# Optimization experiments

Hardware: AMD Instinct MI355X
Metric: run time of the kernel (lower is better)

The kernel has to match this reference:

```python
import jax, jax.numpy as jnp
import numpy as np

B, N, E, T, DIN, H, G, ND, NT, L = 4, 10000, 320000, 16, 16, 64, 64, 16, 3, 7


def _mlp2(x, W1, b1, W2, b2):
    # Linear -> LeakyReLU -> (Dropout: eval identity) -> Linear -> LeakyReLU
    h = jax.nn.leaky_relu(x @ W1 + b1)
    return jax.nn.leaky_relu(h @ W2 + b2)


def _gcn_conv(x, src, dst, ew, nt, W1, b1, W2, b2):
    # x: [B,N,D], nt: [B,N,ND], ew: [*,E,1] broadcastable over batch
    x_in = _mlp2(jnp.concatenate([x, nt], axis=-1), W1, b1, W2, b2)  # [B,N,G]
    msgs = x_in[:, src, :] * ew                                      # gather + weight, [B,E,G]
    aggr = jnp.zeros(x_in.shape, x_in.dtype).at[:, dst, :].add(msgs) # scatter-add, [B,N,G]
    return x + aggr


def _gru(x, Wx, Wh, bx, bh):
    # PyTorch-style GRU over time axis. x: [B,N,T,DIN] -> hs: [T,B,N,H]
    xw = jnp.einsum('bntd,dh->tbnh', x, Wx) + bx  # precompute input projections [T,B,N,3H]
    h0 = jnp.zeros(x.shape[:2] + (Wh.shape[0],), x.dtype)

    def step(h, xw_t):
        hw = h @ Wh + bh
        xr, xz, xn = jnp.split(xw_t, 3, axis=-1)
        hr, hz, hn = jnp.split(hw, 3, axis=-1)
        r = jax.nn.sigmoid(xr + hr)
        z = jax.nn.sigmoid(xz + hz)
        n = jnp.tanh(xn + r * hn)
        h_new = (1 - z) * n + z * h
        return h_new, h_new

    _, hs = jax.lax.scan(step, h0, xw)
    return hs


def reference(input_day, edge_attr, gru_Wx, gru_Wh, gru_bx, gru_bh,
              rnn_fc_W, rnn_fc_b,
              e_emb, e_c0_W1, e_c0_b1, e_c0_W2, e_c0_b2,
              e_c1_W1, e_c1_b1, e_c1_W2, e_c1_b2,
              e_fm_W1, e_fm_b1, e_fm_W2, e_fm_b2,
              g_emb, g_c0_W1, g_c0_b1, g_c0_W2, g_c0_b2,
              g_c1_W1, g_c1_b1, g_c1_W2, g_c1_b2,
              gcn_fc_W, gcn_fc_b,
              edge_index, node_type_ids):
    src, dst = edge_index[0], edge_index[1]

    # KRNN encoder (GRU) + max over time + FC head
    hs = _gru(input_day, gru_Wx, gru_Wh, gru_bx, gru_bh)  # [T,B,N,H]
    rnn_out = hs.max(axis=0)                              # kr_out.max(dim=-2) -> [B,N,H]
    y_rnn = rnn_out @ rnn_fc_W + rnn_fc_b                 # [B,N,L]

    # EdgeNet: GCN stack on static edge_attr, then per-edge pair MLP -> gate
    nt_e = jnp.broadcast_to(e_emb[node_type_ids][None], (B, N, ND))
    ew0 = edge_attr.reshape(1, E, 1)
    x = rnn_out
    x = _gcn_conv(x, src, dst, ew0, nt_e, e_c0_W1, e_c0_b1, e_c0_W2, e_c0_b2)
    x = _gcn_conv(x, src, dst, ew0, nt_e, e_c1_W1, e_c1_b1, e_c1_W2, e_c1_b2)
    edge_x = jnp.concatenate([x[:, src, :], x[:, dst, :]], axis=-1)  # [B,E,2G]
    h = jax.nn.leaky_relu(edge_x @ e_fm_W1 + e_fm_b1)
    edge_gate = jax.nn.relu(h @ e_fm_W2 + e_fm_b2)                   # [B,E,1]

    # Main GCNNet with learned edge gates
    nt_g = jnp.broadcast_to(g_emb[node_type_ids][None], (B, N, ND))
    x = rnn_out
    x = _gcn_conv(x, src, dst, edge_gate, nt_g, g_c0_W1, g_c0_b1, g_c0_W2, g_c0_b2)
    x = _gcn_conv(x, src, dst, edge_gate, nt_g, g_c1_W1, g_c1_b1, g_c1_W2, g_c1_b2)
    y_gcn = x @ gcn_fc_W + gcn_fc_b                                  # [B,N,L]

    return y_rnn + y_gcn


def setup_inputs() -> dict:
    key = jax.random.key(0)
    ks = iter(jax.random.split(key, 48))

    def nrm(shape, s=0.1):
        return jax.random.normal(next(ks), shape, jnp.float32) * s

    inp = {}
    inp['input_day'] = jax.random.normal(next(ks), (B, N, T, DIN), jnp.float32)
    inp['edge_index'] = jax.random.randint(next(ks), (2, E), 0, N)
    inp['node_type_ids'] = jax.random.randint(next(ks), (N,), 0, NT)
    inp['edge_attr'] = jax.random.uniform(next(ks), (E,), jnp.float32)

    inp['gru_Wx'] = nrm((DIN, 3 * H))
    inp['gru_Wh'] = nrm((H, 3 * H))
    inp['gru_bx'] = jnp.zeros((3 * H,), jnp.float32)
    inp['gru_bh'] = jnp.zeros((3 * H,), jnp.float32)
    inp['rnn_fc_W'] = nrm((H, L))
    inp['rnn_fc_b'] = jnp.zeros((L,), jnp.float32)

    inp['e_emb'] = nrm((NT, ND))
    inp['g_emb'] = nrm((NT, ND))
    for pre, in_dim in (('e_c0', H + ND), ('e_c1', G + ND), ('g_c0', H + ND), ('g_c1', G + ND)):
        inp[pre + '_W1'] = nrm((in_dim, G))
        inp[pre + '_b1'] = jnp.zeros((G,), jnp.float32)
        inp[pre + '_W2'] = nrm((G, G))
        inp[pre + '_b2'] = jnp.zeros((G,), jnp.float32)

    inp['e_fm_W1'] = nrm((2 * G, G))
    inp['e_fm_b1'] = jnp.zeros((G,), jnp.float32)
    inp['e_fm_W2'] = nrm((G, 1))
    inp['e_fm_b2'] = jnp.zeros((1,), jnp.float32)

    inp['gcn_fc_W'] = nrm((G, L))
    inp['gcn_fc_b'] = jnp.zeros((L,), jnp.float32)
    return inp
```

## Files before the change

### kernel.cpp

```cpp
#include <hip/hip_runtime.h>
#include <hip/hip_bf16.h>

#define NB 4
#define NN 10000
#define NE 320000
#define BN 40000
#define NL 7

typedef float f32x4 __attribute__((ext_vector_type(4)));
typedef __bf16 bf16x8 __attribute__((ext_vector_type(8)));

__device__ __forceinline__ float bf2f(unsigned short u){
  unsigned x = ((unsigned)u) << 16;
  return __builtin_bit_cast(float, x);
}
__device__ __forceinline__ unsigned short f2bf(float f){
  unsigned u = __builtin_bit_cast(unsigned, f);
  u += 0x7fffu + ((u >> 16) & 1u);
  return (unsigned short)(u >> 16);
}
__device__ __forceinline__ bf16x8 zero8(){
  uint4 z = make_uint4(0u,0u,0u,0u);
  return __builtin_bit_cast(bf16x8, z);
}
__device__ __forceinline__ bf16x8 one8(){
  uint4 z = make_uint4(0x3f80u,0u,0u,0u);
  return __builtin_bit_cast(bf16x8, z);
}
__device__ __forceinline__ bf16x8 ld8bf(const unsigned short* p){
  uint4 u = *(const uint4*)p;
  return __builtin_bit_cast(bf16x8, u);
}
__device__ __forceinline__ unsigned pk2(float lo, float hi){
  unsigned r;
  asm("v_cvt_pk_bf16_f32 %0, %1, %2" : "=v"(r) : "v"(lo), "v"(hi));
  return r;
}
__device__ __forceinline__ bf16x8 ld8f(const float* p){
  float4 a = *(const float4*)p;
  float4 b = *(const float4*)(p+4);
  uint4 u = make_uint4(pk2(a.x,a.y), pk2(a.z,a.w), pk2(b.x,b.y), pk2(b.z,b.w));
  return __builtin_bit_cast(bf16x8, u);
}
__device__ __forceinline__ float frcp(float x){ return __builtin_amdgcn_rcpf(x); }
__device__ __forceinline__ float tanh_(float x){ return 1.f - 2.f*frcp(__expf(2.f*x)+1.f); }
__device__ __forceinline__ float lrelu(float x){ return x > 0.f ? x : 0.01f*x; }

#define LDS_WAIT() asm volatile("s_waitcnt lgkmcnt(0)" ::: "memory")

__device__ __forceinline__ void mlp2_body(
    int bid,
    const float* __restrict__ x,
    const int* __restrict__ ntid,
    const float* __restrict__ emb,
    const float* __restrict__ W1,
    const float* __restrict__ b1,
    const float* __restrict__ W2,
    const float* __restrict__ b2,
    unsigned short* __restrict__ out)
{
  __shared__ __attribute__((aligned(16))) unsigned short W1T[64][96];
  __shared__ __attribute__((aligned(16))) unsigned short W2T[64][72];
  __shared__ __attribute__((aligned(16))) unsigned short hb[4][16][72];
  __shared__ float sb1[64], sb2[64];
  int tid = threadIdx.x;
  for (int i=tid;i<80*64;i+=256){ int k=i>>6, n=i&63; W1T[n][k]=f2bf(W1[i]); }
  for (int i=tid;i<64*16;i+=256){ int n=i>>4, k=80+(i&15); W1T[n][k]=0; }
  for (int i=tid;i<64*64;i+=256){ int k=i>>6, n=i&63; W2T[n][k]=f2bf(W2[i]); }
  if (tid<64){ sb1[tid]=b1[tid]; sb2[tid]=b2[tid]; }
  __syncthreads();

  int wave = tid>>6, lane = tid&63, ln16 = lane&15, quad = lane>>4;
  int row0 = bid*64 + wave*16;
  int r_ = row0 + ln16;
  const float* xr = x + (size_t)r_*64;
  bf16x8 a0 = ld8f(xr + quad*8);
  bf16x8 a1 = ld8f(xr + 32 + quad*8);
  int id = ntid[r_ % NN];
  bf16x8 a2 = (quad<2) ? ld8f(emb + id*16 + quad*8) : zero8();

  f32x4 acc[4];
  #pragma unroll
  for (int nt=0;nt<4;++nt){
    float bb = sb1[nt*16+ln16];
    acc[nt] = (f32x4){bb,bb,bb,bb};
    acc[nt] = __builtin_amdgcn_mfma_f32_16x16x32_bf16(a0, ld8bf(&W1T[nt*16+ln16][quad*8]),    acc[nt], 0,0,0);
    acc[nt] = __builtin_amdgcn_mfma_f32_16x16x32_bf16(a1, ld8bf(&W1T[nt*16+ln16][32+quad*8]), acc[nt], 0,0,0);
    acc[nt] = __builtin_amdgcn_mfma_f32_16x16x32_bf16(a2, ld8bf(&W1T[nt*16+ln16][64+quad*8]), acc[nt], 0,0,0);
  }
  #pragma unroll
  for (int nt=0;nt<4;++nt)
    #pragma unroll
    for (int i=0;i<4;++i)
      hb[wave][quad*4+i][nt*16+ln16] = f2bf(lrelu(acc[nt][i]));
  LDS_WAIT();
  bf16x8 h0 = ld8bf(&hb[wave][ln16][quad*8]);
  bf16x8 h1 = ld8bf(&hb[wave][ln16][32+quad*8]);
  f32x4 acc2[4];
  #pragma unroll
  for (int nt=0;nt<4;++nt){
    float bb = sb2[nt*16+ln16];
    acc2[nt] = (f32x4){bb,bb,bb,bb};
    acc2[nt] = __builtin_amdgcn_mfma_f32_16x16x32_bf16(h0, ld8bf(&W2T[nt*16+ln16][quad*8]),    acc2[nt], 0,0,0);
    acc2[nt] = __builtin_amdgcn_mfma_f32_16x16x32_bf16(h1, ld8bf(&W2T[nt*16+ln16][32+quad*8]), acc2[nt], 0,0,0);
  }
  #pragma unroll
  for (int nt=0;nt<4;++nt)
    #pragma unroll
    for (int i=0;i<4;++i)
      out[(size_t)(row0+quad*4+i)*64 + nt*16+ln16] = f2bf(lrelu(acc2[nt][i]));
}

__global__ __launch_bounds__(256, 2) void gru_count_kernel(
    const float* __restrict__ xd,
    const float* __restrict__ Wx,
    const float* __restrict__ Wh,
    const float* __restrict__ bx,
    const float* __restrict__ bh,
    float* __restrict__ rnn,
    const int* __restrict__ ei,
    int* __restrict__ counts)
{
  if (blockIdx.x >= 625){
    int e = (blockIdx.x-625)*256 + threadIdx.x;
    atomicAdd(&counts[ei[NE+e]], 1);
    return;
  }
  __shared__ __attribute__((aligned(16))) unsigned short WhT[192][72];
  __shared__ __attribute__((aligned(16))) unsigned short WxT[192][40];
  __shared__ __attribute__((aligned(16))) unsigned short hb[4][16][76];
  int tid = threadIdx.x;
  int wave = tid >> 6, lane = tid & 63;
  int ln16 = lane & 15, quad = lane >> 4;

  for (int i = tid; i < 64*192; i += 256){
    int k = i / 192, n = i - k*192;
    WhT[n][k] = f2bf(Wh[i]);
  }
  for (int i = tid; i < 16*192; i += 256){
    int k = i / 192, n = i - k*192;
    WxT[n][k] = f2bf(Wx[i]);
    WxT[n][17+k] = 0;
  }
  if (tid < 192){
    float bias = (tid < 128) ? (bx[tid] + bh[tid]) : bx[tid];
    WxT[tid][16] = f2bf(bias);
  }
  for (int i = tid; i < 4*16*76; i += 256) ((unsigned short*)hb)[i] = 0;
  __syncthreads();

  int rowbase = blockIdx.x * 64 + wave * 16;

  bf16x8 whf[2][12];
  #pragma unroll
  for (int kt=0; kt<2; ++kt)
    #pragma unroll
    for (int nt=0; nt<12; ++nt)
      whf[kt][nt] = ld8bf(&WhT[nt*16 + ln16][kt*32 + quad*8]);

  f32x4 bhn2[4];
  #pragma unroll
  for (int j=0;j<4;++j)
    bhn2[j] = *(const f32x4*)(bh + 128 + j*16 + quad*4);

  f32x4 hprev[4], vmax[4];
  #pragma unroll
  for (int j=0;j<4;++j){
    hprev[j] = (f32x4){0.f,0.f,0.f,0.f};
    vmax[j]  = (f32x4){-1e30f,-1e30f,-1e30f,-1e30f};
  }

  const float* xrow = xd + (size_t)(rowbase + ln16) * 256;
  unsigned short* hrow = &hb[wave][ln16][0];

  bf16x8 axc;
  if (quad < 2) axc = ld8f(xrow + quad*8);
  else          axc = (quad == 2) ? one8() : zero8();

  for (int t = 0; t < 16; ++t){
    bf16x8 axn;
    if (quad < 2) axn = (t < 15) ? ld8f(xrow + (t+1)*16 + quad*8) : zero8();
    else          axn = (quad == 2) ? one8() : zero8();
    bf16x8 ah0 = ld8bf(hrow + quad*8);
    bf16x8 ah1 = ld8bf(hrow + 32 + quad*8);

    #pragma unroll
    for (int j=0;j<4;++j){
      bf16x8 xr = ld8bf(&WxT[j*16+ln16][quad*8]);
      bf16x8 xz = ld8bf(&WxT[(4+j)*16+ln16][quad*8]);
      bf16x8 xn = ld8bf(&WxT[(8+j)*16+ln16][quad*8]);
      f32x4 z4 = (f32x4){0.f,0.f,0.f,0.f};
      f32x4 ar = __builtin_amdgcn_mfma_f32_16x16x32_bf16(xr, axc, z4, 0,0,0);
      ar = __builtin_amdgcn_mfma_f32_16x16x32_bf16(whf[0][j], ah0, ar, 0,0,0);
      ar = __builtin_amdgcn_mfma_f32_16x16x32_bf16(whf[1][j], ah1, ar, 0,0,0);
      f32x4 az = __builtin_amdgcn_mfma_f32_16x16x32_bf16(xz, axc, z4, 0,0,0);
      az = __builtin_amdgcn_mfma_f32_16x16x32_bf16(whf[0][4+j], ah0, az, 0,0,0);
      az = __builtin_amdgcn_mfma_f32_16x16x32_bf16(whf[1][4+j], ah1, az, 0,0,0);
      f32x4 an = __builtin_amdgcn_mfma_f32_16x16x32_bf16(xn, axc, z4, 0,0,0);
      f32x4 ah = __builtin_amdgcn_mfma_f32_16x16x32_bf16(whf[0][8+j], ah0, bhn2[j], 0,0,0);
      ah = __builtin_amdgcn_mfma_f32_16x16x32_bf16(whf[1][8+j], ah1, ah, 0,0,0);
      f32x4 hv;
      #pragma unroll
      for (int i=0;i<4;++i){
        float Er = __expf(-ar[i]);
        float Ez = __expf(-az[i]);
        float pr = 1.f + Er, pz = 1.f + Ez;
        float D  = frcp(pr * pz);
        float r  = D * pz;
        float z  = D * pr;
        float nn = tanh_(an[i] + r * ah[i]);
        float h  = fmaf(z, hprev[j][i]-nn, nn);
        hprev[j][i] = h;
        vmax[j][i] = fmaxf(vmax[j][i], h);
        hv[i] = h;
      }
      *(uint2*)&hb[wave][ln16][j*16+quad*4] = make_uint2(pk2(hv[0],hv[1]), pk2(hv[2],hv[3]));
    }
    LDS_WAIT();
    axc = axn;
  }
  float* orow = rnn + (size_t)(rowbase + ln16)*64;
  #pragma unroll
  for (int j=0;j<4;++j)
    *(f32x4*)(orow + j*16 + quad*4) = vmax[j];
}

__global__ __launch_bounds__(1024) void scan_kernel(const int* __restrict__ counts,
                                                    int* __restrict__ rowptr, int* __restrict__ cursor){
  __shared__ int incl[10240];
  __shared__ int wsum[16];
  int tid=threadIdx.x, wave=tid>>6, lane=tid&63;
  int base = wave*640;
  int carry=0;
  #pragma unroll
  for (int c=0;c<10;++c){
    int i = base + c*64 + lane;
    int v = (i<NN)? counts[i] : 0;
    int s = v;
    #pragma unroll
    for (int off=1;off<64;off<<=1){
      int t_ = __shfl_up(s, off);
      if (lane>=off) s += t_;
    }
    s += carry;
    incl[base + c*64 + lane] = s;
    carry = __shfl(s, 63);
  }
  if (lane==63) wsum[wave]=carry;
  __syncthreads();
  if (wave==0){
    int w_ = (lane<16)? wsum[lane]:0;
    #pragma unroll
    for (int off=1;off<16;off<<=1){
      int t_ = __shfl_up(w_, off);
      if (lane>=off) w_ += t_;
    }
    if (lane<16) wsum[lane]=w_;
  }
  __syncthreads();
  int woff = (wave>0)? wsum[wave-1] : 0;
  #pragma unroll
  for (int c=0;c<10;++c){
    int i = base + c*64 + lane;
    if (i<NN){
      int excl = incl[i] + woff - counts[i];
      rowptr[i]=excl; cursor[i]=excl;
    }
  }
  if (tid==0) rowptr[NN]=wsum[15];
}

__global__ __launch_bounds__(256) void fill_mlp2e_kernel(
    const int* __restrict__ ei,
    const float* __restrict__ ea,
    int* __restrict__ cursor,
    int* __restrict__ ssrc,
    float* __restrict__ wcsr,
    const float* __restrict__ x,
    const int* __restrict__ ntid,
    const float* __restrict__ emb,
    const float* __restrict__ W1, const float* __restrict__ b1,
    const float* __restrict__ W2, const float* __restrict__ b2,
    unsigned short* __restrict__ out)
{
  if (blockIdx.x >= 625){
    int e = (blockIdx.x-625)*256 + threadIdx.x;
    int d = ei[NE+e];
    int pos = atomicAdd(&cursor[d],1);
    ssrc[pos]=ei[e];
    wcsr[pos]=ea[e];
    return;
  }
  mlp2_body(blockIdx.x, x, ntid, emb, W1, b1, W2, b2, out);
}

__global__ __launch_bounds__(256) void aggr_mlp_kernel(
    const float* __restrict__ x,
    const unsigned short* __restrict__ xin,
    const int* __restrict__ rowptr,
    const int* __restrict__ ssrc,
    const float* __restrict__ wp,
    int bstride,
    const int* __restrict__ ntid,
    const float* __restrict__ emb,
    const float* __restrict__ W1,
    const float* __restrict__ b1,
    const float* __restrict__ W2,
    const float* __restrict__ b2,
    float* __restrict__ xe_out,
    unsigned short* __restrict__ out)
{
  int u = blockIdx.x;
  int b = (u & 7) >> 1;
  int m = ((u >> 3) << 1) | (u & 1);
  if (m >= 625) return;
  int row0 = b*NN + m*16;

  __shared__ __attribute__((aligned(16))) unsigned short W1T[64][96];
  __shared__ __attribute__((aligned(16))) unsigned short W2T[64][72];
  __shared__ __attribute__((aligned(16))) unsigned short hb[16][72];
  __shared__ __attribute__((aligned(16))) unsigned short h2[16][72];
  __shared__ float sb1[64], sb2[64];
  int tid = threadIdx.x;
  for (int i=tid;i<80*64;i+=256){ int k=i>>6, n=i&63; W1T[n][k]=f2bf(W1[i]); }
  for (int i=tid;i<64*16;i+=256){ int n=i>>4, k=80+(i&15); W1T[n][k]=0; }
  for (int i=tid;i<64*64;i+=256){ int k=i>>6, n=i&63; W2T[n][k]=f2bf(W2[i]); }
  if (tid<64){ sb1[tid]=b1[tid]; sb2[tid]=b2[tid]; }

  int wave = tid>>6, lane = tid&63, ln16 = lane&15, quad = lane>>4;
  int r = wave*4 + quad;
  int row = row0 + r;
  int n = m*16 + r;
  int l = ln16;
  int p0 = rowptr[n], p1 = rowptr[n+1];
  const unsigned short* xb_ = xin + (size_t)b*NN*64;
  const float* wb = wp + (size_t)b*bstride;
  float a0=0.f, a1=0.f, a2=0.f, a3=0.f;
  #pragma unroll 4
  for (int p=p0; p<p1; ++p){
    int s = ssrc[p];
    float w = wb[p];
    uint2 mm = *(const uint2*)(xb_ + (size_t)s*64 + l*4);
    a0 += bf2f((unsigned short)(mm.x & 0xffffu)) * w;
    a1 += bf2f((unsigned short)(mm.x >> 16)) * w;
    a2 += bf2f((unsigned short)(mm.y & 0xffffu)) * w;
    a3 += bf2f((unsigned short)(mm.y >> 16)) * w;
  }
  float4 base = *(const float4*)(x + (size_t)row*64 + l*4);
  float o0=base.x+a0, o1=base.y+a1, o2=base.z+a2, o3=base.w+a3;
  float4 ov; ov.x=o0; ov.y=o1; ov.z=o2; ov.w=o3;
  *(float4*)(xe_out + (size_t)row*64 + l*4) = ov;
  *(uint2*)&hb[r][l*4] = make_uint2(pk2(o0,o1), pk2(o2,o3));
  __syncthreads();

  int id = ntid[m*16 + ln16];
  bf16x8 xa0 = ld8bf(&hb[ln16][quad*8]);
  bf16x8 xa1 = ld8bf(&hb[ln16][32+quad*8]);
  bf16x8 xa2 = (quad<2) ? ld8f(emb + id*16 + quad*8) : zero8();
  float bb = sb1[wave*16+ln16];
  f32x4 acc = (f32x4){bb,bb,bb,bb};
  acc = __builtin_amdgcn_mfma_f32_16x16x32_bf16(xa0, ld8bf(&W1T[wave*16+ln16][quad*8]),    acc, 0,0,0);
  acc = __builtin_amdgcn_mfma_f32_16x16x32_bf16(xa1, ld8bf(&W1T[wave*16+ln16][32+quad*8]), acc, 0,0,0);
  acc = __builtin_amdgcn_mfma_f32_16x16x32_bf16(xa2, ld8bf(&W1T[wave*16+ln16][64+quad*8]), acc, 0,0,0);
  #pragma unroll
  for (int i=0;i<4;++i)
    h2[quad*4+i][wave*16+ln16] = f2bf(lrelu(acc[i]));
  __syncthreads();
  bf16x8 hh0 = ld8bf(&h2[ln16][quad*8]);
  bf16x8 hh1 = ld8bf(&h2[ln16][32+quad*8]);
  float b2v = sb2[wave*16+ln16];
  f32x4 acc2 = (f32x4){b2v,b2v,b2v,b2v};
  acc2 = __builtin_amdgcn_mfma_f32_16x16x32_bf16(hh0, ld8bf(&W2T[wave*16+ln16][quad*8]),    acc2, 0,0,0);
  acc2 = __builtin_amdgcn_mfma_f32_16x16x32_bf16(hh1, ld8bf(&W2T[wave*16+ln16][32+quad*8]), acc2, 0,0,0);
  #pragma unroll
  for (int i=0;i<4;++i)
    out[(size_t)(row0+quad*4+i)*64 + wave*16+ln16] = f2bf(lrelu(acc2[i]));
}

__global__ __launch_bounds__(256) void aggr_uv_kernel(
    const float* __restrict__ x,
    const unsigned short* __restrict__ xin,
    const int* __restrict__ rowptr,
    const int* __restrict__ ssrc,
    const float* __restrict__ wp,
    int bstride,
    const float* __restrict__ W1,
    unsigned short* __restrict__ uvp)
{
  int u = blockIdx.x;
  int b = (u & 7) >> 1;
  int m = ((u >> 3) << 1) | (u & 1);
  if (m >= 625) return;
  int row0 = b*NN + m*16;

  __shared__ __attribute__((aligned(16))) unsigned short WT[128][72];
  __shared__ __attribute__((aligned(16))) unsigned short hb[16][72];
  int tid = threadIdx.x;
  for (int i=tid;i<64*64;i+=256){
    int k=i>>6, n=i&63;
    WT[n][k]    = f2bf(W1[i]);
    WT[64+n][k] = f2bf(W1[64*64 + i]);
  }

  int wave = tid>>6, lane = tid&63, ln16 = lane&15, quad = lane>>4;
  int r = wave*4 + quad;
  int row = row0 + r;
  int n = m*16 + r;
  int l = ln16;
  int p0 = rowptr[n], p1 = rowptr[n+1];
  const unsigned short* xb_ = xin + (size_t)b*NN*64;
  const float* wb = wp + (size_t)b*bstride;
  float a0=0.f, a1=0.f, a2=0.f, a3=0.f;
  #pragma unroll 4
  for (int p=p0; p<p1; ++p){
    int s = ssrc[p];
    float w = wb[p];
    uint2 mm = *(const uint2*)(xb_ + (size_t)s*64 + l*4);
    a0 += bf2f((unsigned short)(mm.x & 0xffffu)) * w;
    a1 += bf2f((unsigned short)(mm.x >> 16)) * w;
    a2 += bf2f((unsigned short)(mm.y & 0xffffu)) * w;
    a3 += bf2f((unsigned short)(mm.y >> 16)) * w;
  }
  float4 base = *(const float4*)(x + (size_t)row*64 + l*4);
  float o0=base.x+a0, o1=base.y+a1, o2=base.z+a2, o3=base.w+a3;
  *(uint2*)&hb[r][l*4] = make_uint2(pk2(o0,o1), pk2(o2,o3));
  __syncthreads();

  bf16x8 xa0 = ld8bf(&hb[ln16][quad*8]);
  bf16x8 xa1 = ld8bf(&hb[ln16][32+quad*8]);
  #pragma unroll
  for (int t=0;t<2;++t){
    int nt = wave*2 + t;
    f32x4 acc = (f32x4){0.f,0.f,0.f,0.f};
    acc = __builtin_amdgcn_mfma_f32_16x16x32_bf16(xa0, ld8bf(&WT[nt*16+ln16][quad*8]),    acc, 0,0,0);
    acc = __builtin_amdgcn_mfma_f32_16x16x32_bf16(xa1, ld8bf(&WT[nt*16+ln16][32+quad*8]), acc, 0,0,0);
    #pragma unroll
    for (int i=0;i<4;++i)
      uvp[(size_t)(row0+quad*4+i)*128 + nt*16+ln16] = f2bf(acc[i]);
  }
}

__global__ __launch_bounds__(256) void gate_mlp2g_kernel(
    const unsigned short* __restrict__ uvp,
    const int* __restrict__ rowptr,
    const int* __restrict__ ssrc,
    const float* __restrict__ b1,
    const float* __restrict__ W2g,
    const float* __restrict__ b2,
    float* __restrict__ gate,
    const float* __restrict__ x,
    const int* __restrict__ ntid,
    const float* __restrict__ emb,
    const float* __restrict__ mW1, const float* __restrict__ mb1,
    const float* __restrict__ mW2, const float* __restrict__ mb2,
    unsigned short* __restrict__ mout)
{
  if (blockIdx.x < 625){
    mlp2_body(blockIdx.x, x, ntid, emb, mW1, mb1, mW2, mb2, mout);
    return;
  }
  int u = blockIdx.x;
  int b = (u & 7) >> 1;
  int m = (((u - 625) >> 3) << 1) | (u & 1);
  if (m >= 2500) return;
  int tid=threadIdx.x;
  int wave=tid>>6, lane=tid&63;
  int sub=lane>>4, l=lane&15;
  int n = m*4 + wave;
  int p0 = rowptr[n], p1 = rowptr[n+1];
  const unsigned short* ub = uvp + (size_t)b*NN*128;
  uint2 vu = *(const uint2*)(ub + (size_t)n*128 + 64 + l*4);
  float v0=bf2f((unsigned short)(vu.x&0xffffu)), v1=bf2f((unsigned short)(vu.x>>16));
  float v2=bf2f((unsigned short)(vu.y&0xffffu)), v3=bf2f((unsigned short)(vu.y>>16));
  float4 bb = *(const float4*)(b1 + l*4);
  float4 ww = *(const float4*)(W2g + l*4);
  float b2v = b2[0];
  float* gb = gate + (size_t)b*NE;
  #pragma unroll 4
  for (int p=p0+sub; p<p1; p+=4){
    int s = ssrc[p];
    uint2 uu = *(const uint2*)(ub + (size_t)s*128 + l*4);
    float h0 = lrelu(bf2f((unsigned short)(uu.x&0xffffu)) + v0 + bb.x);
    float h1 = lrelu(bf2f((unsigned short)(uu.x>>16))     + v1 + bb.y);
    float h2 = lrelu(bf2f((unsigned short)(uu.y&0xffffu)) + v2 + bb.z);
    float h3 = lrelu(bf2f((unsigned short)(uu.y>>16))     + v3 + bb.w);
    float part = h0*ww.x + h1*ww.y + h2*ww.z + h3*ww.w;
    part += __shfl_xor(part,1);
    part += __shfl_xor(part,2);
    part += __shfl_xor(part,4);
    part += __shfl_xor(part,8);
    if (l==0){
      float g = part + b2v;
      gb[p] = g>0.f ? g : 0.f;
    }
  }
}

__global__ __launch_bounds__(256) void aggr_final_kernel(
    const float* x,
    const unsigned short* __restrict__ xin,
    const int* __restrict__ rowptr,
    const int* __restrict__ ssrc,
    const float* __restrict__ wp,
    const float* __restrict__ rnn,
    const float* __restrict__ Wr, const float* __restrict__ br,
    const float* __restrict__ Wg, const float* __restrict__ bg,
    float* __restrict__ out)
{
  int u = blockIdx.x;
  int b = (u & 7) >> 1;
  int m = ((u >> 3) << 1) | (u & 1);
  if (m >= 2500) return;

  __shared__ float sWr[448], sWg[448], sb[7];
  int tid=threadIdx.x;
  for (int i=tid;i<448;i+=256){ sWr[i]=Wr[i]; sWg[i]=Wg[i]; }
  if (tid<7) sb[tid]=br[tid]+bg[tid];
  __syncthreads();
  int wave=tid>>6, lane=tid&63;
  int sub=lane>>4, l=lane&15;
  int n = m*4 + wave;
  int bid = b*NN + n;
  int p0 = rowptr[n], p1 = rowptr[n+1];
  const unsigned short* xb_ = xin + (size_t)b*NN*64;
  const float* wb = wp + (size_t)b*NE;
  float a0=0.f, a1=0.f, a2=0.f, a3=0.f;
  #pragma unroll 4
  for (int p=p0+sub; p<p1; p+=4){
    int s = ssrc[p];
    float w = wb[p];
    uint2 mm = *(const uint2*)(xb_ + (size_t)s*64 + l*4);
    a0 += bf2f((unsigned short)(mm.x & 0xffffu)) * w;
    a1 += bf2f((unsigned short)(mm.x >> 16)) * w;
    a2 += bf2f((unsigned short)(mm.y & 0xffffu)) * w;
    a3 += bf2f((unsigned short)(mm.y >> 16)) * w;
  }
  a0 += __shfl_xor(a0,16); a0 += __shfl_xor(a0,32);
  a1 += __shfl_xor(a1,16); a1 += __shfl_xor(a1,32);
  a2 += __shfl_xor(a2,16); a2 += __shfl_xor(a2,32);
  a3 += __shfl_xor(a3,16); a3 += __shfl_xor(a3,32);
  if (sub==0){
    float4 base = *(const float4*)(x + (size_t)bid*64 + l*4);
    float o0=base.x+a0, o1=base.y+a1, o2=base.z+a2, o3=base.w+a3;
    float4 rr = *(const float4*)(rnn + (size_t)bid*64 + l*4);
    float part[7];
    #pragma unroll
    for (int q=0;q<7;++q)
      part[q] = o0*sWg[(l*4+0)*7+q] + o1*sWg[(l*4+1)*7+q]
              + o2*sWg[(l*4+2)*7+q] + o3*sWg[(l*4+3)*7+q]
              + rr.x*sWr[(l*4+0)*7+q] + rr.y*sWr[(l*4+1)*7+q]
              + rr.z*sWr[(l*4+2)*7+q] + rr.w*sWr[(l*4+3)*7+q];
    #pragma unroll
    for (int q=0;q<7;++q){
      part[q] += __shfl_xor(part[q],1);
      part[q] += __shfl_xor(part[q],2);
      part[q] += __shfl_xor(part[q],4);
      part[q] += __shfl_xor(part[q],8);
    }
    if (l==0){
      #pragma unroll
      for (int q=0;q<7;++q) out[(size_t)bid*7+q] = part[q] + sb[q];
    }
  }
}

extern "C" void kernel_launch(void* const* d_in, const int* in_sizes, int n_in,
                              void* d_out, int out_size, void* d_ws, size_t ws_size,
                              hipStream_t stream)
{
  (void)in_sizes; (void)n_in; (void)out_size; (void)ws_size;
  const float* input_day = (const float*)d_in[0];
  const int* ei    = (const int*)d_in[1];
  const int* ntid  = (const int*)d_in[2];
  const float* edge_attr = (const float*)d_in[3];
  const float* gWx = (const float*)d_in[4];
  const float* gWh = (const float*)d_in[5];
  const float* gbx = (const float*)d_in[6];
  const float* gbh = (const float*)d_in[7];
  const float* rW  = (const float*)d_in[8];
  const float* rb  = (const float*)d_in[9];
  const float* eemb= (const float*)d_in[10];
  const float* gemb= (const float*)d_in[11];
  const float* ec0W1=(const float*)d_in[12];
  const float* ec0b1=(const float*)d_in[13];
  const float* ec0W2=(const float*)d_in[14];
  const float* ec0b2=(const float*)d_in[15];
  const float* ec1W1=(const float*)d_in[16];
  const float* ec1b1=(const float*)d_in[17];
  const float* ec1W2=(const float*)d_in[18];
  const float* ec1b2=(const float*)d_in[19];
  const float* gc0W1=(const float*)d_in[20];
  const float* gc0b1=(const float*)d_in[21];
  const float* gc0W2=(const float*)d_in[22];
  const float* gc0b2=(const float*)d_in[23];
  const float* gc1W1=(const float*)d_in[24];
  const float* gc1b1=(const float*)d_in[25];
  const float* gc1W2=(const float*)d_in[26];
  const float* gc1b2=(const float*)d_in[27];
  const float* efmW1=(const float*)d_in[28];
  const float* efmb1=(const float*)d_in[29];
  const float* efmW2=(const float*)d_in[30];
  const float* efmb2=(const float*)d_in[31];
  const float* gcnW =(const float*)d_in[32];
  const float* gcnb =(const float*)d_in[33];

  char* ws = (char*)d_ws;
  float*          rnn = (float*)(ws);
  float*          xe  = (float*)(ws + 10240000);
  unsigned short* xinA= (unsigned short*)(ws + 20480000);
  unsigned short* uvp = (unsigned short*)(ws + 25600000);
  float*          gat = (float*)(ws + 35840000);
  int* rowptr= (int*)(ws + 40960000);
  int* cursor= (int*)(ws + 41000064);
  int* counts= (int*)(ws + 41040064);
  int*   ssrc= (int*)(ws + 41080064);
  float* wcsr= (float*)(ws + 42360064);
  unsigned short* xinB = (unsigned short*)gat;
  unsigned short* xinD = (unsigned short*)uvp;

  hipMemsetAsync(counts, 0, NN*sizeof(int), stream);
  gru_count_kernel<<<1875, 256, 0, stream>>>(input_day, gWx, gWh, gbx, gbh, rnn,
                                             ei, counts);
  scan_kernel<<<1, 1024, 0, stream>>>(counts, rowptr, cursor);
  fill_mlp2e_kernel<<<1875, 256, 0, stream>>>(ei, edge_attr, cursor, ssrc, wcsr,
                                              rnn, ntid, eemb,
                                              ec0W1, ec0b1, ec0W2, ec0b2, xinA);
  aggr_mlp_kernel<<<2504, 256, 0, stream>>>(rnn, xinA, rowptr, ssrc, wcsr, 0,
                                            ntid, eemb, ec1W1, ec1b1, ec1W2, ec1b2,
                                            xe, xinB);
  aggr_uv_kernel<<<2504, 256, 0, stream>>>(xe, xinB, rowptr, ssrc, wcsr, 0,
                                           efmW1, uvp);
  gate_mlp2g_kernel<<<10633, 256, 0, stream>>>(uvp, rowptr, ssrc,
                                               efmb1, efmW2, efmb2, gat,
                                               rnn, ntid, gemb,
                                               gc0W1, gc0b1, gc0W2, gc0b2, xinA);
  aggr_mlp_kernel<<<2504, 256, 0, stream>>>(rnn, xinA, rowptr, ssrc, gat, NE,
                                            ntid, gemb, gc1W1, gc1b1, gc1W2, gc1b2,
                                            xe, xinD);
  aggr_final_kernel<<<10008, 256, 0, stream>>>(xe, xinD, rowptr, ssrc, gat, rnn,
                                               rW, rb, gcnW, gcnb, (float*)d_out);
}
```

Before: 440.5 us.

## Pretransform MLP weights to bf16 once and read them from global memory

Extra blocks in the GRU kernel now convert and transpose every MLP weight matrix into bf16 once, writing them into a scratch area that reuses the output buffer. The MLP and aggregation kernels drop their per-block LDS staging and the __syncthreads that went with it, and read weights and biases straight from global memory (L2/L1-cached). This removes thousands of redundant per-block fp32-to-bf16 transposes and frees LDS to raise occupancy. In exchange, MFMA operands are now fetched with global loads instead of LDS reads, and the scratch area relies on d_out not being written until the final kernel.

```diff
diff --git a/kernel.cpp b/kernel.cpp
--- a/kernel.cpp
+++ b/kernel.cpp
@@ -48,28 +48,23 @@
 
 #define LDS_WAIT() asm volatile("s_waitcnt lgkmcnt(0)" ::: "memory")
 
+#define WT_SET   10240
+#define WT_UV    40960
+#define WT_TOTAL 49152
+
 __device__ __forceinline__ void mlp2_body(
     int bid,
     const float* __restrict__ x,
     const int* __restrict__ ntid,
     const float* __restrict__ emb,
-    const float* __restrict__ W1,
+    const unsigned short* __restrict__ W1T,
     const float* __restrict__ b1,
-    const float* __restrict__ W2,
+    const unsigned short* __restrict__ W2T,
     const float* __restrict__ b2,
     unsigned short* __restrict__ out)
 {
-  __shared__ __attribute__((aligned(16))) unsigned short W1T[64][96];
-  __shared__ __attribute__((aligned(16))) unsigned short W2T[64][72];
   __shared__ __attribute__((aligned(16))) unsigned short hb[4][16][72];
-  __shared__ float sb1[64], sb2[64];
   int tid = threadIdx.x;
-  for (int i=tid;i<80*64;i+=256){ int k=i>>6, n=i&63; W1T[n][k]=f2bf(W1[i]); }
-  for (int i=tid;i<64*16;i+=256){ int n=i>>4, k=80+(i&15); W1T[n][k]=0; }
-  for (int i=tid;i<64*64;i+=256){ int k=i>>6, n=i&63; W2T[n][k]=f2bf(W2[i]); }
-  if (tid<64){ sb1[tid]=b1[tid]; sb2[tid]=b2[tid]; }
-  __syncthreads();
-
   int wave = tid>>6, lane = tid&63, ln16 = lane&15, quad = lane>>4;
   int row0 = bid*64 + wave*16;
   int r_ = row0 + ln16;
@@ -82,11 +77,11 @@
   f32x4 acc[4];
   #pragma unroll
   for (int nt=0;nt<4;++nt){
-    float bb = sb1[nt*16+ln16];
+    float bb = b1[nt*16+ln16];
     acc[nt] = (f32x4){bb,bb,bb,bb};
-    acc[nt] = __builtin_amdgcn_mfma_f32_16x16x32_bf16(a0, ld8bf(&W1T[nt*16+ln16][quad*8]),    acc[nt], 0,0,0);
-    acc[nt] = __builtin_amdgcn_mfma_f32_16x16x32_bf16(a1, ld8bf(&W1T[nt*16+ln16][32+quad*8]), acc[nt], 0,0,0);
-    acc[nt] = __builtin_amdgcn_mfma_f32_16x16x32_bf16(a2, ld8bf(&W1T[nt*16+ln16][64+quad*8]), acc[nt], 0,0,0);
+    acc[nt] = __builtin_amdgcn_mfma_f32_16x16x32_bf16(a0, ld8bf(W1T + (nt*16+ln16)*96 + quad*8),      acc[nt], 0,0,0);
+    acc[nt] = __builtin_amdgcn_mfma_f32_16x16x32_bf16(a1, ld8bf(W1T + (nt*16+ln16)*96 + 32 + quad*8), acc[nt], 0,0,0);
+    acc[nt] = __builtin_amdgcn_mfma_f32_16x16x32_bf16(a2, ld8bf(W1T + (nt*16+ln16)*96 + 64 + quad*8), acc[nt], 0,0,0);
   }
   #pragma unroll
   for (int nt=0;nt<4;++nt)
@@ -99,10 +94,10 @@
   f32x4 acc2[4];
   #pragma unroll
   for (int nt=0;nt<4;++nt){
-    float bb = sb2[nt*16+ln16];
+    float bb = b2[nt*16+ln16];
     acc2[nt] = (f32x4){bb,bb,bb,bb};
-    acc2[nt] = __builtin_amdgcn_mfma_f32_16x16x32_bf16(h0, ld8bf(&W2T[nt*16+ln16][quad*8]),    acc2[nt], 0,0,0);
-    acc2[nt] = __builtin_amdgcn_mfma_f32_16x16x32_bf16(h1, ld8bf(&W2T[nt*16+ln16][32+quad*8]), acc2[nt], 0,0,0);
+    acc2[nt] = __builtin_amdgcn_mfma_f32_16x16x32_bf16(h0, ld8bf(W2T + (nt*16+ln16)*64 + quad*8),      acc2[nt], 0,0,0);
+    acc2[nt] = __builtin_amdgcn_mfma_f32_16x16x32_bf16(h1, ld8bf(W2T + (nt*16+ln16)*64 + 32 + quad*8), acc2[nt], 0,0,0);
   }
   #pragma unroll
   for (int nt=0;nt<4;++nt)
@@ -119,8 +114,39 @@
     const float* __restrict__ bh,
     float* __restrict__ rnn,
     const int* __restrict__ ei,
-    int* __restrict__ counts)
-{
+    int* __restrict__ counts,
+    const float* __restrict__ ec0W1, const float* __restrict__ ec0W2,
+    const float* __restrict__ ec1W1, const float* __restrict__ ec1W2,
+    const float* __restrict__ gc0W1, const float* __restrict__ gc0W2,
+    const float* __restrict__ gc1W1, const float* __restrict__ gc1W2,
+    const float* __restrict__ efmW1,
+    unsigned short* __restrict__ wt)
+{
+  if (blockIdx.x >= 1875){
+    int pidx = blockIdx.x - 1875;
+    for (int i = pidx*256 + threadIdx.x; i < WT_TOTAL; i += 2048){
+      unsigned short v;
+      if (i < WT_UV){
+        int s = i / WT_SET, j = i - s*WT_SET;
+        const float* W1s = (s==0) ? ec0W1 : (s==1) ? ec1W1 : (s==2) ? gc0W1 : gc1W1;
+        const float* W2s = (s==0) ? ec0W2 : (s==1) ? ec1W2 : (s==2) ? gc0W2 : gc1W2;
+        if (j < 6144){
+          int n = j / 96, k = j - n*96;
+          v = (k < 80) ? f2bf(W1s[k*64+n]) : (unsigned short)0;
+        } else {
+          int j2 = j - 6144;
+          int n = j2 >> 6, k = j2 & 63;
+          v = f2bf(W2s[k*64+n]);
+        }
+      } else {
+        int j = i - WT_UV;
+        int n = j >> 6, k = j & 63;
+        v = f2bf((n < 64) ? efmW1[k*64+n] : efmW1[4096 + k*64 + (n-64)]);
+      }
+      wt[i] = v;
+    }
+    return;
+  }
   if (blockIdx.x >= 625){
     int e = (blockIdx.x-625)*256 + threadIdx.x;
     atomicAdd(&counts[ei[NE+e]], 1);
@@ -279,8 +305,8 @@
     const float* __restrict__ x,
     const int* __restrict__ ntid,
     const float* __restrict__ emb,
-    const float* __restrict__ W1, const float* __restrict__ b1,
-    const float* __restrict__ W2, const float* __restrict__ b2,
+    const unsigned short* __restrict__ wt,
+    const float* __restrict__ b1, const float* __restrict__ b2,
     unsigned short* __restrict__ out)
 {
   if (blockIdx.x >= 625){
@@ -291,7 +317,7 @@
     wcsr[pos]=ea[e];
     return;
   }
-  mlp2_body(blockIdx.x, x, ntid, emb, W1, b1, W2, b2, out);
+  mlp2_body(blockIdx.x, x, ntid, emb, wt, b1, wt + 6144, b2, out);
 }
 
 __global__ __launch_bounds__(256) void aggr_mlp_kernel(
@@ -303,9 +329,9 @@
     int bstride,
     const int* __restrict__ ntid,
     const float* __restrict__ emb,
-    const float* __restrict__ W1,
+    const unsigned short* __restrict__ W1T,
     const float* __restrict__ b1,
-    const float* __restrict__ W2,
+    const unsigned short* __restrict__ W2T,
     const float* __restrict__ b2,
     float* __restrict__ xe_out,
     unsigned short* __restrict__ out)
@@ -316,17 +342,9 @@
   if (m >= 625) return;
   int row0 = b*NN + m*16;
 
-  __shared__ __attribute__((aligned(16))) unsigned short W1T[64][96];
-  __shared__ __attribute__((aligned(16))) unsigned short W2T[64][72];
   __shared__ __attribute__((aligned(16))) unsigned short hb[16][72];
   __shared__ __attribute__((aligned(16))) unsigned short h2[16][72];
-  __shared__ float sb1[64], sb2[64];
   int tid = threadIdx.x;
-  for (int i=tid;i<80*64;i+=256){ int k=i>>6, n=i&63; W1T[n][k]=f2bf(W1[i]); }
-  for (int i=tid;i<64*16;i+=256){ int n=i>>4, k=80+(i&15); W1T[n][k]=0; }
-  for (int i=tid;i<64*64;i+=256){ int k=i>>6, n=i&63; W2T[n][k]=f2bf(W2[i]); }
-  if (tid<64){ sb1[tid]=b1[tid]; sb2[tid]=b2[tid]; }
-
   int wave = tid>>6, lane = tid&63, ln16 = lane&15, quad = lane>>4;
   int r = wave*4 + quad;
   int row = row0 + r;
@@ -357,21 +375,21 @@
   bf16x8 xa0 = ld8bf(&hb[ln16][quad*8]);
   bf16x8 xa1 = ld8bf(&hb[ln16][32+quad*8]);
   bf16x8 xa2 = (quad<2) ? ld8f(emb + id*16 + quad*8) : zero8();
-  float bb = sb1[wave*16+ln16];
+  float bb = b1[wave*16+ln16];
   f32x4 acc = (f32x4){bb,bb,bb,bb};
-  acc = __builtin_amdgcn_mfma_f32_16x16x32_bf16(xa0, ld8bf(&W1T[wave*16+ln16][quad*8]),    acc, 0,0,0);
-  acc = __builtin_amdgcn_mfma_f32_16x16x32_bf16(xa1, ld8bf(&W1T[wave*16+ln16][32+quad*8]), acc, 0,0,0);
-  acc = __builtin_amdgcn_mfma_f32_16x16x32_bf16(xa2, ld8bf(&W1T[wave*16+ln16][64+quad*8]), acc, 0,0,0);
+  acc = __builtin_amdgcn_mfma_f32_16x16x32_bf16(xa0, ld8bf(W1T + (wave*16+ln16)*96 + quad*8),      acc, 0,0,0);
+  acc = __builtin_amdgcn_mfma_f32_16x16x32_bf16(xa1, ld8bf(W1T + (wave*16+ln16)*96 + 32 + quad*8), acc, 0,0,0);
+  acc = __builtin_amdgcn_mfma_f32_16x16x32_bf16(xa2, ld8bf(W1T + (wave*16+ln16)*96 + 64 + quad*8), acc, 0,0,0);
   #pragma unroll
   for (int i=0;i<4;++i)
     h2[quad*4+i][wave*16+ln16] = f2bf(lrelu(acc[i]));
   __syncthreads();
   bf16x8 hh0 = ld8bf(&h2[ln16][quad*8]);
   bf16x8 hh1 = ld8bf(&h2[ln16][32+quad*8]);
-  float b2v = sb2[wave*16+ln16];
+  float b2v = b2[wave*16+ln16];
   f32x4 acc2 = (f32x4){b2v,b2v,b2v,b2v};
-  acc2 = __builtin_amdgcn_mfma_f32_16x16x32_bf16(hh0, ld8bf(&W2T[wave*16+ln16][quad*8]),    acc2, 0,0,0);
-  acc2 = __builtin_amdgcn_mfma_f32_16x16x32_bf16(hh1, ld8bf(&W2T[wave*16+ln16][32+quad*8]), acc2, 0,0,0);
+  acc2 = __builtin_amdgcn_mfma_f32_16x16x32_bf16(hh0, ld8bf(W2T + (wave*16+ln16)*64 + quad*8),      acc2, 0,0,0);
+  acc2 = __builtin_amdgcn_mfma_f32_16x16x32_bf16(hh1, ld8bf(W2T + (wave*16+ln16)*64 + 32 + quad*8), acc2, 0,0,0);
   #pragma unroll
   for (int i=0;i<4;++i)
     out[(size_t)(row0+quad*4+i)*64 + wave*16+ln16] = f2bf(lrelu(acc2[i]));
@@ -384,7 +402,7 @@
     const int* __restrict__ ssrc,
     const float* __restrict__ wp,
     int bstride,
-    const float* __restrict__ W1,
+    const unsigned short* __restrict__ WT,
     unsigned short* __restrict__ uvp)
 {
   int u = blockIdx.x;
@@ -393,15 +411,8 @@
   if (m >= 625) return;
   int row0 = b*NN + m*16;
 
-  __shared__ __attribute__((aligned(16))) unsigned short WT[128][72];
   __shared__ __attribute__((aligned(16))) unsigned short hb[16][72];
   int tid = threadIdx.x;
-  for (int i=tid;i<64*64;i+=256){
-    int k=i>>6, n=i&63;
-    WT[n][k]    = f2bf(W1[i]);
-    WT[64+n][k] = f2bf(W1[64*64 + i]);
-  }
-
   int wave = tid>>6, lane = tid&63, ln16 = lane&15, quad = lane>>4;
   int r = wave*4 + quad;
   int row = row0 + r;
@@ -432,8 +443,8 @@
   for (int t=0;t<2;++t){
     int nt = wave*2 + t;
     f32x4 acc = (f32x4){0.f,0.f,0.f,0.f};
-    acc = __builtin_amdgcn_mfma_f32_16x16x32_bf16(xa0, ld8bf(&WT[nt*16+ln16][quad*8]),    acc, 0,0,0);
-    acc = __builtin_amdgcn_mfma_f32_16x16x32_bf16(xa1, ld8bf(&WT[nt*16+ln16][32+quad*8]), acc, 0,0,0);
+    acc = __builtin_amdgcn_mfma_f32_16x16x32_bf16(xa0, ld8bf(WT + (nt*16+ln16)*64 + quad*8),      acc, 0,0,0);
+    acc = __builtin_amdgcn_mfma_f32_16x16x32_bf16(xa1, ld8bf(WT + (nt*16+ln16)*64 + 32 + quad*8), acc, 0,0,0);
     #pragma unroll
     for (int i=0;i<4;++i)
       uvp[(size_t)(row0+quad*4+i)*128 + nt*16+ln16] = f2bf(acc[i]);
@@ -451,12 +462,12 @@
     const float* __restrict__ x,
     const int* __restrict__ ntid,
     const float* __restrict__ emb,
-    const float* __restrict__ mW1, const float* __restrict__ mb1,
-    const float* __restrict__ mW2, const float* __restrict__ mb2,
+    const unsigned short* __restrict__ wtg,
+    const float* __restrict__ mb1, const float* __restrict__ mb2,
     unsigned short* __restrict__ mout)
 {
   if (blockIdx.x < 625){
-    mlp2_body(blockIdx.x, x, ntid, emb, mW1, mb1, mW2, mb2, mout);
+    mlp2_body(blockIdx.x, x, ntid, emb, wtg, mb1, wtg + 6144, mb2, mout);
     return;
   }
   int u = blockIdx.x;
@@ -617,25 +628,31 @@
   float* wcsr= (float*)(ws + 42360064);
   unsigned short* xinB = (unsigned short*)gat;
   unsigned short* xinD = (unsigned short*)uvp;
+  unsigned short* wt   = (unsigned short*)d_out;
 
   hipMemsetAsync(counts, 0, NN*sizeof(int), stream);
-  gru_count_kernel<<<1875, 256, 0, stream>>>(input_day, gWx, gWh, gbx, gbh, rnn,
-                                             ei, counts);
+  gru_count_kernel<<<1883, 256, 0, stream>>>(input_day, gWx, gWh, gbx, gbh, rnn,
+                                             ei, counts,
+                                             ec0W1, ec0W2, ec1W1, ec1W2,
+                                             gc0W1, gc0W2, gc1W1, gc1W2,
+                                             efmW1, wt);
   scan_kernel<<<1, 1024, 0, stream>>>(counts, rowptr, cursor);
   fill_mlp2e_kernel<<<1875, 256, 0, stream>>>(ei, edge_attr, cursor, ssrc, wcsr,
                                               rnn, ntid, eemb,
-                                              ec0W1, ec0b1, ec0W2, ec0b2, xinA);
+                                              wt, ec0b1, ec0b2, xinA);
   aggr_mlp_kernel<<<2504, 256, 0, stream>>>(rnn, xinA, rowptr, ssrc, wcsr, 0,
-                                            ntid, eemb, ec1W1, ec1b1, ec1W2, ec1b2,
+                                            ntid, eemb,
+                                            wt + WT_SET, ec1b1, wt + WT_SET + 6144, ec1b2,
                                             xe, xinB);
   aggr_uv_kernel<<<2504, 256, 0, stream>>>(xe, xinB, rowptr, ssrc, wcsr, 0,
-                                           efmW1, uvp);
+                                           wt + WT_UV, uvp);
   gate_mlp2g_kernel<<<10633, 256, 0, stream>>>(uvp, rowptr, ssrc,
                                                efmb1, efmW2, efmb2, gat,
                                                rnn, ntid, gemb,
-                                               gc0W1, gc0b1, gc0W2, gc0b2, xinA);
+                                               wt + 2*WT_SET, gc0b1, gc0b2, xinA);
   aggr_mlp_kernel<<<2504, 256, 0, stream>>>(rnn, xinA, rowptr, ssrc, gat, NE,
-                                            ntid, gemb, gc1W1, gc1b1, gc1W2, gc1b2,
+                                            ntid, gemb,
+                                            wt + 3*WT_SET, gc1b1, wt + 3*WT_SET + 6144, gc1b2,
                                             xe, xinD);
   aggr_final_kernel<<<10008, 256, 0, stream>>>(xe, xinD, rowptr, ssrc, gat, rnn,
                                                rW, rb, gcnW, gcnb, (float*)d_out);
```

Result: faster. 419.2 us, median of 2 (-4.8%).
